# Performance work log

Hardware: AMD Instinct MI355X
Metric: run time of the kernel (lower is better)

## Reference

```python
import jax, jax.numpy as jnp
import numpy as np

N = 50000      # neurons
R = 4          # receptors per neuron
D = 5          # max delay steps
N_IN = 17400   # input (LGN) channels
B = 2
T = 50
E_REC = 2000000
E_IN = 500000
DT = 1.0
SIGMA = 0.5    # gauss_std
DAMP = 0.3     # dampening_factor


@jax.custom_vjp
def spike_gauss(v):
    return (v > 0).astype(v.dtype)

def _sg_fwd(v):
    return (v > 0).astype(v.dtype), v

def _sg_bwd(v, g):
    return (g * jnp.exp(-(v * v) / (SIGMA * SIGMA)) * DAMP,)

spike_gauss.defvjp(_sg_fwd, _sg_bwd)


def _constrained(w):
    # Dale's law: sign buffer is fixed (stop_gradient), values clipped to keep sign
    s = jax.lax.stop_gradient(jnp.sign(w))
    return jnp.where(s >= 0, jax.nn.relu(w), -jax.nn.relu(-w))


def setup_inputs() -> dict:
    ks = jax.random.split(jax.random.key(0), 20)
    x = jax.random.uniform(ks[0], (B, T, N_IN), jnp.float32)
    rest = jax.random.randint(ks[1], (T, B), 0, 11).astype(jnp.int32)  # Binomial(10,0.1) count
    rec_rows = jax.random.randint(ks[2], (E_REC,), 0, R * N).astype(jnp.int32)
    rec_cols = jax.random.randint(ks[3], (E_REC,), 0, D * N).astype(jnp.int32)
    rec_w = jax.random.normal(ks[4], (E_REC,), jnp.float32) * 1e-3
    in_rows = jax.random.randint(ks[5], (E_IN,), 0, R * N).astype(jnp.int32)
    in_cols = jax.random.randint(ks[6], (E_IN,), 0, N_IN).astype(jnp.int32)
    in_w = jax.random.normal(ks[7], (E_IN,), jnp.float32) * 1e-3
    bkg = jax.random.normal(ks[8], (N * R,), jnp.float32) * 0.1
    # per-neuron params, already in normalized voltage units (offset=E_L, scale=V_th-E_L)
    v_th = jnp.ones((N,), jnp.float32)
    e_l = jnp.zeros((N,), jnp.float32)
    v_reset = jax.random.uniform(ks[9], (N,), jnp.float32, -0.2, 0.0)
    g = jax.random.uniform(ks[10], (N,), jnp.float32, 4.0, 6.0)
    c_m = jax.random.uniform(ks[11], (N,), jnp.float32, 100.0, 200.0)
    tau = c_m / g
    decay = jnp.exp(-DT / tau)
    current_factor = (1.0 - decay) * tau / c_m
    t_ref = jnp.full((N,), 2.0, jnp.float32)
    asc_amps = jax.random.normal(ks[12], (N, 2), jnp.float32) * 0.01
    param_k = jax.random.uniform(ks[13], (N, 2), jnp.float32, 0.1, 0.5)
    tau_syn = jax.random.uniform(ks[14], (N, R), jnp.float32, 2.0, 10.0)
    syn_decay = jnp.exp(-DT / tau_syn)
    psc_initial = jnp.asarray(np.e, jnp.float32) / tau_syn
    voltage_scale = jax.random.uniform(ks[15], (N,), jnp.float32, 20.0, 30.0)
    voltage_offset = jnp.full((N,), -70.0, jnp.float32)
    return dict(x=x, rec_w=rec_w, in_w=in_w, bkg=bkg, v_th=v_th, e_l=e_l,
                v_reset=v_reset, g=g, t_ref=t_ref, asc_amps=asc_amps,
                param_k=param_k, decay=decay, current_factor=current_factor,
                syn_decay=syn_decay, psc_initial=psc_initial,
                voltage_scale=voltage_scale, voltage_offset=voltage_offset,
                rec_rows=rec_rows, rec_cols=rec_cols, in_rows=in_rows,
                in_cols=in_cols, rest=rest)


def _forward(x, rec_w, in_w, bkg, v_th, e_l, v_reset, g, t_ref, asc_amps,
             param_k, decay, current_factor, syn_decay, psc_initial,
             voltage_scale, voltage_offset, rec_rows, rec_cols, in_rows,
             in_cols, rest):
    rec_wc = _constrained(rec_w)
    in_wc = _constrained(in_w)
    asc_decay = jnp.exp(-DT * param_k)   # (N,2)
    leak = g * e_l                       # (N,)
    normalizer = v_th - e_l              # (N,)

    z_buf0 = jnp.zeros((B, D, N), jnp.float32)  # delay line, slot 0 = most recent
    v0 = jnp.broadcast_to(v_reset, (B, N))
    zN = jnp.zeros((B, N), jnp.float32)
    zNR = jnp.zeros((B, N, R), jnp.float32)
    carry0 = (z_buf0, v0, zN, zN, zN, zNR, zNR)

    xs = (jnp.transpose(x, (1, 0, 2)), rest)  # (T,B,N_IN), (T,B)

    def step(carry, inp):
        x_t, rest_t = inp
        z_buf, v, r, a1, a2, psc_rise, psc = carry
        # input projection: sparse COO (R*N, N_IN) matvec per batch via gather + scatter-add
        cur = jnp.zeros((B, R * N), jnp.float32).at[:, in_rows].add(x_t[:, in_cols] * in_wc[None, :])
        cur = cur + bkg[None, :] * (rest_t.astype(jnp.float32)[:, None] / 10.0)
        prev_z = z_buf[:, 0]
        zb_flat = z_buf.reshape(B, D * N)
        # recurrent sparse COO (R*N, D*N) matvec over the delay buffer
        i_rec = jnp.zeros((B, R * N), jnp.float32).at[:, rec_rows].add(zb_flat[:, rec_cols] * rec_wc[None, :])
        rec_in = (i_rec + cur).reshape(B, N, R)
        new_psc_rise = syn_decay[None] * psc_rise + rec_in * psc_initial[None]
        new_psc = psc * syn_decay[None] + DT * syn_decay[None] * psc_rise
        new_r = jax.nn.relu(r + prev_z * t_ref[None] - DT)
        new_a1 = asc_decay[:, 0][None] * a1 + prev_z * asc_amps[:, 0][None]
        new_a2 = asc_decay[:, 1][None] * a2 + prev_z * asc_amps[:, 1][None]
        reset_current = prev_z * (v_reset - v_th)[None]
        input_current = psc.sum(-1)  # uses OLD psc, matching the torch code
        new_v = decay[None] * v + current_factor[None] * (input_current + a1 + a2 + leak[None]) + reset_current
        v_sc = (new_v - v_th[None]) / normalizer[None]
        new_z = spike_gauss(v_sc)
        new_z = jnp.where(new_r > 0.0, jnp.zeros_like(new_z), new_z)
        new_z_buf = jnp.concatenate([new_z[:, None, :], z_buf[:, :-1]], axis=1)
        v_out = new_v * voltage_scale[None] + voltage_offset[None]
        new_carry = (new_z_buf, new_v, new_r, new_a1, new_a2, new_psc_rise, new_psc)
        return new_carry, (new_z, v_out)

    _, (zs, vs) = jax.lax.scan(step, carry0, xs)
    return jnp.transpose(zs, (1, 0, 2)), jnp.transpose(vs, (1, 0, 2))  # (B,T,N) each


def reference(x, rec_w, in_w, bkg, v_th, e_l, v_reset, g, t_ref, asc_amps,
              param_k, decay, current_factor, syn_decay, psc_initial,
              voltage_scale, voltage_offset, rec_rows, rec_cols, in_rows,
              in_cols, rest):
    return _forward(x, rec_w, in_w, bkg, v_th, e_l, v_reset, g, t_ref,
                    asc_amps, param_k, decay, current_factor, syn_decay,
                    psc_initial, voltage_scale, voltage_offset, rec_rows,
                    rec_cols, in_rows, in_cols, rest)
```

## Files before the change

kernel.cpp:

```cpp
#include <hip/hip_runtime.h>

#define NN    50000
#define RR    4
#define DDEP  5
#define NIN   17400
#define BB    2
#define TT    50
#define EREC  2000000
#define EIN   500000
#define RNN   (RR*NN)
#define DNN   (DDEP*NN)
#define RING  6
#define TB    (TT*BB)
#define CH    20
#define NCH   (TB/CH)
#define SCAN_TPB 256
#define SCAN_ITEMS 4

struct SP {
  const float* x; const float* bkg;
  const float* v_th; const float* e_l; const float* v_reset; const float* g;
  const float* t_ref; const float* asc_amps; const float* param_k;
  const float* decay; const float* cf; const float* syn_decay; const float* psc_init;
  const float* vscale; const float* voff;
  const int* rest;
  float* out_z; float* out_v;
  float* cur_ring;
  int*   flags;
  int*   bar;
  const int* row_ptr;
  const int2* cw_in;
  const int* col_ptr;
  const int2* cw_rec;
  const float* in_cur;
};

__global__ void hist2_k(const int* __restrict__ in_rows, const int* __restrict__ rec_cols,
                        int* __restrict__ cnt_in, int* __restrict__ cnt_rec) {
  int i = blockIdx.x * blockDim.x + threadIdx.x;
  int nth = gridDim.x * blockDim.x;
  for (int e = i; e < EIN + EREC; e += nth) {
    if (e < EIN) atomicAdd(&cnt_in[in_rows[e]], 1);
    else         atomicAdd(&cnt_rec[rec_cols[e - EIN]], 1);
  }
}

__global__ __launch_bounds__(SCAN_TPB) void blocksum_k(const int* __restrict__ cnt, int n,
                                                       int* __restrict__ partial) {
  __shared__ int sm[SCAN_TPB];
  int base = (blockIdx.x * SCAN_TPB + threadIdx.x) * SCAN_ITEMS;
  int s = 0;
  #pragma unroll
  for (int j = 0; j < SCAN_ITEMS; ++j) { int idx = base + j; if (idx < n) s += cnt[idx]; }
  sm[threadIdx.x] = s; __syncthreads();
  for (int off = SCAN_TPB / 2; off > 0; off >>= 1) {
    if (threadIdx.x < off) sm[threadIdx.x] += sm[threadIdx.x + off];
    __syncthreads();
  }
  if (threadIdx.x == 0) partial[blockIdx.x] = sm[0];
}

__global__ __launch_bounds__(SCAN_TPB) void scanpart_k(int* __restrict__ partial, int nb) {
  __shared__ int sm[SCAN_TPB];
  int i = threadIdx.x;
  int v = (i < nb) ? partial[i] : 0;
  sm[i] = v; __syncthreads();
  for (int off = 1; off < SCAN_TPB; off <<= 1) {
    int a = (i >= off) ? sm[i - off] : 0;
    __syncthreads();
    sm[i] += a;
    __syncthreads();
  }
  if (i < nb) partial[i] = sm[i] - v;
}

__global__ __launch_bounds__(SCAN_TPB) void finalize_k(const int* __restrict__ cnt, int n,
                                                       const int* __restrict__ partial,
                                                       int* __restrict__ ptr,
                                                       int* __restrict__ cursor, int nE) {
  __shared__ int sm[SCAN_TPB];
  int tidl = threadIdx.x;
  int base = (blockIdx.x * SCAN_TPB + tidl) * SCAN_ITEMS;
  int local[SCAN_ITEMS];
  int s = 0;
  #pragma unroll
  for (int j = 0; j < SCAN_ITEMS; ++j) {
    int idx = base + j;
    int c = (idx < n) ? cnt[idx] : 0;
    local[j] = c; s += c;
  }
  sm[tidl] = s; __syncthreads();
  for (int off = 1; off < SCAN_TPB; off <<= 1) {
    int a = (tidl >= off) ? sm[tidl - off] : 0;
    __syncthreads();
    sm[tidl] += a;
    __syncthreads();
  }
  int run = partial[blockIdx.x] + sm[tidl] - s;
  #pragma unroll
  for (int j = 0; j < SCAN_ITEMS; ++j) {
    int idx = base + j;
    if (idx < n) { ptr[idx] = run; cursor[idx] = run; run += local[j]; }
  }
  if (blockIdx.x == 0 && tidl == 0) ptr[n] = nE;
}

__global__ void scatter2_k(const int* __restrict__ in_rows, const int* __restrict__ in_cols,
                           const float* __restrict__ in_w,
                           const int* __restrict__ rec_cols, const int* __restrict__ rec_rows,
                           const float* __restrict__ rec_w,
                           int* __restrict__ cur_in, int* __restrict__ cur_rec,
                           int2* __restrict__ cw_in, int2* __restrict__ cw_rec) {
  int i = blockIdx.x * blockDim.x + threadIdx.x;
  int nth = gridDim.x * blockDim.x;
  for (int e = i; e < EIN + EREC; e += nth) {
    if (e < EIN) {
      int pos = atomicAdd(&cur_in[in_rows[e]], 1);
      cw_in[pos] = make_int2(in_cols[e], __float_as_int(in_w[e]));
    } else {
      int ee = e - EIN;
      int pos = atomicAdd(&cur_rec[rec_cols[ee]], 1);
      cw_rec[pos] = make_int2(rec_rows[ee], __float_as_int(rec_w[ee]));
    }
  }
}

__global__ __launch_bounds__(256) void xpose_k(const float* __restrict__ x,
                                               float* __restrict__ xT) {
  __shared__ float tile[64][TB + 1];
  int c0 = blockIdx.x * 64;
  int cl = threadIdx.x & 63;
  for (int tb = threadIdx.x >> 6; tb < TB; tb += 4) {
    int t = tb >> 1, b = tb & 1;
    int c = c0 + cl;
    tile[cl][tb] = (c < NIN) ? x[((size_t)b * TT + t) * NIN + c] : 0.f;
  }
  __syncthreads();
  int cc = threadIdx.x >> 2;
  int seg = (threadIdx.x & 3) * (TB / 4);
  int c = c0 + cc;
  if (c < NIN) {
    for (int j = seg; j < seg + TB / 4; ++j)
      xT[(size_t)c * TB + j] = tile[cc][j];
  }
}

__global__ __launch_bounds__(256) void precomp2_k(const float* __restrict__ xT,
                                                  const int* __restrict__ rest,
                                                  const float* __restrict__ bkg,
                                                  const int* __restrict__ row_ptr,
                                                  const int2* __restrict__ cw,
                                                  float* __restrict__ ic) {
  const int nbn = (NN + 255) >> 8;
  int chunk = blockIdx.x / nbn;
  int n = (blockIdx.x % nbn) * 256 + threadIdx.x;
  if (n >= NN) return;
  const int tb0 = chunk * CH;

  float restf[CH];
  #pragma unroll
  for (int j = 0; j < CH; ++j) restf[j] = (float)rest[tb0 + j] * 0.1f;

  int rp[RR + 1];
  #pragma unroll
  for (int r = 0; r <= RR; ++r) rp[r] = row_ptr[n * RR + r];

  float acc[RR][CH];
  #pragma unroll
  for (int r = 0; r < RR; ++r) {
    float bk = bkg[n * RR + r];
    #pragma unroll
    for (int j = 0; j < CH; ++j) acc[r][j] = bk * restf[j];
    for (int e = rp[r]; e < rp[r + 1]; ++e) {
      int2 c = cw[e];
      float w = __int_as_float(c.y);
      const float* xr = xT + (size_t)c.x * TB + tb0;
      #pragma unroll
      for (int j = 0; j < CH; ++j) acc[r][j] += w * xr[j];
    }
  }
  #pragma unroll
  for (int j = 0; j < CH; ++j) {
    *(float4*)(ic + (size_t)(tb0 + j) * RNN + (size_t)n * RR) =
        make_float4(acc[0][j], acc[1][j], acc[2][j], acc[3][j]);
  }
}

__device__ __forceinline__ void gridbar(int* bar, int nb, int target) {
  __syncthreads();
  if (threadIdx.x == 0) {
    int* cnt = bar;
    int* gen = bar + 32;
    int old = __hip_atomic_fetch_add(cnt, 1, __ATOMIC_ACQ_REL, __HIP_MEMORY_SCOPE_AGENT);
    if (old == nb - 1) {
      __hip_atomic_store(cnt, 0, __ATOMIC_RELAXED, __HIP_MEMORY_SCOPE_AGENT);
      __hip_atomic_store(gen, target, __ATOMIC_RELEASE, __HIP_MEMORY_SCOPE_AGENT);
    } else {
      while (__hip_atomic_load(gen, __ATOMIC_RELAXED, __HIP_MEMORY_SCOPE_AGENT) < target)
        __builtin_amdgcn_s_sleep(1);
      (void)__hip_atomic_load(gen, __ATOMIC_ACQUIRE, __HIP_MEMORY_SCOPE_AGENT);
    }
  }
  __syncthreads();
}

__global__ __launch_bounds__(1024, 1) void snn_all(SP p) {
  const int tid = blockIdx.x * blockDim.x + threadIdx.x;
  const int nb = gridDim.x;

  const bool owner = tid < BB * NN;
  int b = 0, n = 0;
  float sd[RR], pi[RR], bkgv[RR], psc_rise[RR], psc[RR];
  int rbeg[RR], rend[RR];
  float v = 0.f, refr = 0.f, a1 = 0.f, a2 = 0.f, my_z = 0.f;
  float dcy = 0.f, cfac = 0.f, trf = 0.f, amp1 = 0.f, amp2 = 0.f;
  float ad1 = 0.f, ad2 = 0.f, vth = 0.f, invn = 0.f, leak = 0.f;
  float vrst = 0.f, vsc = 0.f, vof = 0.f;
  #pragma unroll
  for (int r = 0; r < RR; ++r) {
    sd[r]=0.f; pi[r]=0.f; bkgv[r]=0.f; psc_rise[r]=0.f; psc[r]=0.f;
    rbeg[r]=0; rend[r]=0;
  }

  if (owner) {
    b = (tid >= NN) ? 1 : 0;
    n = tid - b * NN;
    #pragma unroll
    for (int r = 0; r < RR; ++r) {
      sd[r] = p.syn_decay[n*RR + r];
      pi[r] = p.psc_init[n*RR + r];
    }
    if (!p.in_cur) {
      #pragma unroll
      for (int r = 0; r < RR; ++r) {
        bkgv[r] = p.bkg[n*RR + r];
        rbeg[r] = p.row_ptr[n*RR + r];
        rend[r] = p.row_ptr[n*RR + r + 1];
      }
    }
    vth  = p.v_th[n];
    float el = p.e_l[n];
    invn = 1.0f / (vth - el);
    leak = p.g[n] * el;
    vrst = p.v_reset[n];
    v    = vrst;
    dcy  = p.decay[n];
    cfac = p.cf[n];
    trf  = p.t_ref[n];
    amp1 = p.asc_amps[2*n+0];
    amp2 = p.asc_amps[2*n+1];
    ad1  = expf(-p.param_k[2*n+0]);
    ad2  = expf(-p.param_k[2*n+1]);
    vsc  = p.vscale[n];
    vof  = p.voff[n];
  }
  const float* xb = p.x + (size_t)b * TT * NIN;
  float* ringB = p.cur_ring + (size_t)b * RING * RNN;

  float4 iv = make_float4(0.f, 0.f, 0.f, 0.f);
  if (owner && p.in_cur)
    iv = *(const float4*)(p.in_cur + (size_t)b * RNN + (size_t)n * RR);

  for (int t = 0; t < TT; ++t) {
    if (t) gridbar(p.bar, nb, t);

    if (owner) {
      int slot = t % RING;
      float4* slotR = (float4*)(ringB + (size_t)slot * RNN);
      float4 rv = slotR[n];
      int flag = p.flags[b*RING + slot];

      float rin[RR];
      if (p.in_cur) {
        rin[0] = iv.x; rin[1] = iv.y; rin[2] = iv.z; rin[3] = iv.w;
        if (t + 1 < TT)
          iv = *(const float4*)(p.in_cur + (size_t)((t+1)*BB + b) * RNN + (size_t)n * RR);
      } else {
        float restf = (float)p.rest[t*BB + b] * 0.1f;
        const float* xt = xb + (size_t)t * NIN;
        #pragma unroll
        for (int r = 0; r < RR; ++r) {
          float acc = bkgv[r] * restf;
          for (int e = rbeg[r]; e < rend[r]; ++e) {
            int2 cw = p.cw_in[e];
            acc += xt[cw.x] * __int_as_float(cw.y);
          }
          rin[r] = acc;
        }
      }

      if (flag == t)
        slotR[n] = make_float4(0.f, 0.f, 0.f, 0.f);
      rin[0] += rv.x; rin[1] += rv.y; rin[2] += rv.z; rin[3] += rv.w;

      float prev_z = my_z;
      float input_current = psc[0] + psc[1] + psc[2] + psc[3];
      float new_v = dcy * v + cfac * (input_current + a1 + a2 + leak)
                    + prev_z * (vrst - vth);
      #pragma unroll
      for (int r = 0; r < RR; ++r) {
        float npsc = psc[r] * sd[r] + sd[r] * psc_rise[r];
        psc_rise[r] = sd[r] * psc_rise[r] + rin[r] * pi[r];
        psc[r] = npsc;
      }
      refr = fmaxf(refr + prev_z * trf - 1.0f, 0.f);
      a1 = ad1 * a1 + prev_z * amp1;
      a2 = ad2 * a2 + prev_z * amp2;
      v = new_v;
      float v_scaled = (new_v - vth) * invn;
      float z = (v_scaled > 0.f) ? 1.f : 0.f;
      if (refr > 0.f) z = 0.f;
      my_z = z;
      size_t oidx = (size_t)b * (TT*NN) + (size_t)t * NN + n;
      p.out_z[oidx] = z;
      p.out_v[oidx] = new_v * vsc + vof;

      if (z != 0.f) {
        #pragma unroll
        for (int d = 0; d < DDEP; ++d) {
          int tt = t + 1 + d;
          if (tt >= TT) break;
          int col = d * NN + n;
          int be = p.col_ptr[col], en = p.col_ptr[col + 1];
          if (be != en) {
            int ws_ = tt % RING;
            p.flags[b*RING + ws_] = tt;
            float* ringW = ringB + (size_t)ws_ * RNN;
            for (int e = be; e < en; ++e) {
              int2 cw = p.cw_rec[e];
              atomicAdd(&ringW[cw.x], __int_as_float(cw.y));
            }
          }
        }
      }
    }
  }
}

extern "C" void kernel_launch(void* const* d_in, const int* in_sizes, int n_in,
                              void* d_out, int out_size, void* d_ws, size_t ws_size,
                              hipStream_t stream) {
  SP p;
  p.x        = (const float*)d_in[0];
  const float* rec_w = (const float*)d_in[1];
  const float* in_w  = (const float*)d_in[2];
  p.bkg      = (const float*)d_in[3];
  p.v_th     = (const float*)d_in[4];
  p.e_l      = (const float*)d_in[5];
  p.v_reset  = (const float*)d_in[6];
  p.g        = (const float*)d_in[7];
  p.t_ref    = (const float*)d_in[8];
  p.asc_amps = (const float*)d_in[9];
  p.param_k  = (const float*)d_in[10];
  p.decay    = (const float*)d_in[11];
  p.cf       = (const float*)d_in[12];
  p.syn_decay= (const float*)d_in[13];
  p.psc_init = (const float*)d_in[14];
  p.vscale   = (const float*)d_in[15];
  p.voff     = (const float*)d_in[16];
  const int* rec_rows = (const int*)d_in[17];
  const int* rec_cols = (const int*)d_in[18];
  const int* in_rows  = (const int*)d_in[19];
  const int* in_cols  = (const int*)d_in[20];
  p.rest     = (const int*)d_in[21];
  p.out_z = (float*)d_out;
  p.out_v = (float*)d_out + (size_t)BB * TT * NN;

  char* ws = (char*)d_ws;
  size_t off = 0;
  auto alloc = [&](size_t bytes) { void* q = ws + off; off += (bytes + 255) & ~(size_t)255; return q; };
  float* cur_ring = (float*)alloc(sizeof(float) * (size_t)BB * RING * RNN);
  int*   flags    = (int*)  alloc(sizeof(int) * BB * RING);
  int*   bar      = (int*)  alloc(sizeof(int) * 64);
  int*   row_ptr  = (int*)  alloc(sizeof(int) * ((size_t)RNN + 1));
  int*   col_ptr  = (int*)  alloc(sizeof(int) * ((size_t)DNN + 1));
  int*   cnt_in   = (int*)  alloc(sizeof(int) * (size_t)RNN);
  int*   cnt_rec  = (int*)  alloc(sizeof(int) * (size_t)DNN);
  int*   cur_in   = (int*)  alloc(sizeof(int) * (size_t)RNN);
  int*   cur_rec  = (int*)  alloc(sizeof(int) * (size_t)DNN);
  int*   part_in  = (int*)  alloc(sizeof(int) * SCAN_TPB);
  int*   part_rec = (int*)  alloc(sizeof(int) * SCAN_TPB);
  int2*  cw_in    = (int2*) alloc(sizeof(int2) * (size_t)EIN);
  int2*  cw_rec   = (int2*) alloc(sizeof(int2) * (size_t)EREC);
  float* xT       = (float*)alloc(sizeof(float) * (size_t)NIN * TB);
  float* in_cur   = (float*)alloc(sizeof(float) * (size_t)TB * RNN);
  const bool use_pre = (off <= ws_size);

  p.cur_ring = cur_ring; p.flags = flags; p.bar = bar;
  p.row_ptr = row_ptr; p.cw_in = cw_in;
  p.col_ptr = col_ptr; p.cw_rec = cw_rec;
  p.in_cur = use_pre ? in_cur : nullptr;

  hipMemsetAsync(cur_ring, 0, sizeof(float) * (size_t)BB * RING * RNN, stream);
  hipMemsetAsync(flags, 0xFF, sizeof(int) * BB * RING, stream);
  hipMemsetAsync(bar, 0, sizeof(int) * 64, stream);
  hipMemsetAsync(cnt_in, 0, sizeof(int) * (size_t)RNN, stream);
  hipMemsetAsync(cnt_rec, 0, sizeof(int) * (size_t)DNN, stream);

  hipLaunchKernelGGL(hist2_k, dim3(1024), dim3(256), 0, stream,
                     in_rows, rec_cols, cnt_in, cnt_rec);

  const int NB_IN  = (RNN + SCAN_TPB * SCAN_ITEMS - 1) / (SCAN_TPB * SCAN_ITEMS);
  const int NB_REC = (DNN + SCAN_TPB * SCAN_ITEMS - 1) / (SCAN_TPB * SCAN_ITEMS);
  hipLaunchKernelGGL(blocksum_k, dim3(NB_IN),  dim3(SCAN_TPB), 0, stream, cnt_in,  RNN, part_in);
  hipLaunchKernelGGL(blocksum_k, dim3(NB_REC), dim3(SCAN_TPB), 0, stream, cnt_rec, DNN, part_rec);
  hipLaunchKernelGGL(scanpart_k, dim3(1), dim3(SCAN_TPB), 0, stream, part_in,  NB_IN);
  hipLaunchKernelGGL(scanpart_k, dim3(1), dim3(SCAN_TPB), 0, stream, part_rec, NB_REC);
  hipLaunchKernelGGL(finalize_k, dim3(NB_IN),  dim3(SCAN_TPB), 0, stream, cnt_in,  RNN, part_in,  row_ptr, cur_in,  EIN);
  hipLaunchKernelGGL(finalize_k, dim3(NB_REC), dim3(SCAN_TPB), 0, stream, cnt_rec, DNN, part_rec, col_ptr, cur_rec, EREC);

  hipLaunchKernelGGL(scatter2_k, dim3(1024), dim3(256), 0, stream,
                     in_rows, in_cols, in_w, rec_cols, rec_rows, rec_w,
                     cur_in, cur_rec, cw_in, cw_rec);

  if (use_pre) {
    hipLaunchKernelGGL(xpose_k, dim3((NIN + 63) / 64), dim3(256), 0, stream, p.x, xT);
    const int nbn = (NN + 255) / 256;
    hipLaunchKernelGGL(precomp2_k, dim3(nbn * NCH), dim3(256), 0, stream,
                       xT, p.rest, p.bkg, row_ptr, cw_in, in_cur);
  }

  void* args[] = { (void*)&p };
  hipLaunchCooperativeKernel(reinterpret_cast<const void*>(&snn_all),
                             dim3(104), dim3(1024), args, 0u, stream);
}
```

Baseline: 841.4 us.

## Use hierarchical tree grid barrier and merge scan/memset launches

Replaces the flat single-counter grid barrier with a two-level tree: eight leaf counters each gather 13 blocks, then leaf leaders meet at a root counter and release their group through per-group generation flags. This is meant to cut atomic contention on one cache line at each of the 49 timestep barriers. It also fuses the paired scan kernels into one launch each using a 2D grid, and merges several memsets into one contiguous memset. The tree adds an extra round-trip of latency per barrier in exchange for less contention.

```diff
diff --git a/kernel.cpp b/kernel.cpp
--- a/kernel.cpp
+++ b/kernel.cpp
@@ -14,6 +14,9 @@
 #define TB    (TT*BB)
 #define CH    20
 #define NCH   (TB/CH)
+#define NBLK  104
+#define NXG   8
+#define GSZ   (NBLK/NXG)
 #define SCAN_TPB 256
 #define SCAN_ITEMS 4
 
@@ -45,8 +48,15 @@
   }
 }
 
-__global__ __launch_bounds__(SCAN_TPB) void blocksum_k(const int* __restrict__ cnt, int n,
-                                                       int* __restrict__ partial) {
+__global__ __launch_bounds__(SCAN_TPB) void blocksum2_k(const int* __restrict__ cnt_in,
+                                                        const int* __restrict__ cnt_rec,
+                                                        int* __restrict__ part_in,
+                                                        int* __restrict__ part_rec) {
+  const int n = blockIdx.y ? DNN : RNN;
+  const int* cnt = blockIdx.y ? cnt_rec : cnt_in;
+  int* partial = blockIdx.y ? part_rec : part_in;
+  const int nb = (n + SCAN_TPB * SCAN_ITEMS - 1) / (SCAN_TPB * SCAN_ITEMS);
+  if ((int)blockIdx.x >= nb) return;
   __shared__ int sm[SCAN_TPB];
   int base = (blockIdx.x * SCAN_TPB + threadIdx.x) * SCAN_ITEMS;
   int s = 0;
@@ -60,7 +70,11 @@
   if (threadIdx.x == 0) partial[blockIdx.x] = sm[0];
 }
 
-__global__ __launch_bounds__(SCAN_TPB) void scanpart_k(int* __restrict__ partial, int nb) {
+__global__ __launch_bounds__(SCAN_TPB) void scanpart2_k(int* __restrict__ part_in,
+                                                        int* __restrict__ part_rec) {
+  const int n = blockIdx.x ? DNN : RNN;
+  int* partial = blockIdx.x ? part_rec : part_in;
+  const int nb = (n + SCAN_TPB * SCAN_ITEMS - 1) / (SCAN_TPB * SCAN_ITEMS);
   __shared__ int sm[SCAN_TPB];
   int i = threadIdx.x;
   int v = (i < nb) ? partial[i] : 0;
@@ -74,10 +88,22 @@
   if (i < nb) partial[i] = sm[i] - v;
 }
 
-__global__ __launch_bounds__(SCAN_TPB) void finalize_k(const int* __restrict__ cnt, int n,
-                                                       const int* __restrict__ partial,
-                                                       int* __restrict__ ptr,
-                                                       int* __restrict__ cursor, int nE) {
+__global__ __launch_bounds__(SCAN_TPB) void finalize2_k(const int* __restrict__ cnt_in,
+                                                        const int* __restrict__ cnt_rec,
+                                                        const int* __restrict__ part_in,
+                                                        const int* __restrict__ part_rec,
+                                                        int* __restrict__ ptr_in,
+                                                        int* __restrict__ ptr_rec,
+                                                        int* __restrict__ cur_in,
+                                                        int* __restrict__ cur_rec) {
+  const int n = blockIdx.y ? DNN : RNN;
+  const int nE = blockIdx.y ? EREC : EIN;
+  const int* cnt = blockIdx.y ? cnt_rec : cnt_in;
+  const int* partial = blockIdx.y ? part_rec : part_in;
+  int* ptr = blockIdx.y ? ptr_rec : ptr_in;
+  int* cursor = blockIdx.y ? cur_rec : cur_in;
+  const int nb = (n + SCAN_TPB * SCAN_ITEMS - 1) / (SCAN_TPB * SCAN_ITEMS);
+  if ((int)blockIdx.x >= nb) return;
   __shared__ int sm[SCAN_TPB];
   int tidl = threadIdx.x;
   int base = (blockIdx.x * SCAN_TPB + tidl) * SCAN_ITEMS;
@@ -186,19 +212,31 @@
   }
 }
 
-__device__ __forceinline__ void gridbar(int* bar, int nb, int target) {
+__device__ __forceinline__ void gridbar(int* bar, int target) {
   __syncthreads();
   if (threadIdx.x == 0) {
-    int* cnt = bar;
-    int* gen = bar + 32;
-    int old = __hip_atomic_fetch_add(cnt, 1, __ATOMIC_ACQ_REL, __HIP_MEMORY_SCOPE_AGENT);
-    if (old == nb - 1) {
-      __hip_atomic_store(cnt, 0, __ATOMIC_RELAXED, __HIP_MEMORY_SCOPE_AGENT);
-      __hip_atomic_store(gen, target, __ATOMIC_RELEASE, __HIP_MEMORY_SCOPE_AGENT);
+    const int g = blockIdx.x & (NXG - 1);
+    int* leafCnt = bar + g * 32;
+    int* rootCnt = bar + NXG * 32;
+    int* rootGen = bar + (NXG + 1) * 32;
+    int* leafGen = bar + (NXG + 2 + g) * 32;
+    int lo = __hip_atomic_fetch_add(leafCnt, 1, __ATOMIC_ACQ_REL, __HIP_MEMORY_SCOPE_AGENT);
+    if (lo == GSZ - 1) {
+      __hip_atomic_store(leafCnt, 0, __ATOMIC_RELAXED, __HIP_MEMORY_SCOPE_AGENT);
+      int ro = __hip_atomic_fetch_add(rootCnt, 1, __ATOMIC_ACQ_REL, __HIP_MEMORY_SCOPE_AGENT);
+      if (ro == NXG - 1) {
+        __hip_atomic_store(rootCnt, 0, __ATOMIC_RELAXED, __HIP_MEMORY_SCOPE_AGENT);
+        __hip_atomic_store(rootGen, target, __ATOMIC_RELEASE, __HIP_MEMORY_SCOPE_AGENT);
+      } else {
+        while (__hip_atomic_load(rootGen, __ATOMIC_RELAXED, __HIP_MEMORY_SCOPE_AGENT) < target)
+          __builtin_amdgcn_s_sleep(1);
+        (void)__hip_atomic_load(rootGen, __ATOMIC_ACQUIRE, __HIP_MEMORY_SCOPE_AGENT);
+      }
+      __hip_atomic_store(leafGen, target, __ATOMIC_RELEASE, __HIP_MEMORY_SCOPE_AGENT);
     } else {
-      while (__hip_atomic_load(gen, __ATOMIC_RELAXED, __HIP_MEMORY_SCOPE_AGENT) < target)
+      while (__hip_atomic_load(leafGen, __ATOMIC_RELAXED, __HIP_MEMORY_SCOPE_AGENT) < target)
         __builtin_amdgcn_s_sleep(1);
-      (void)__hip_atomic_load(gen, __ATOMIC_ACQUIRE, __HIP_MEMORY_SCOPE_AGENT);
+      (void)__hip_atomic_load(leafGen, __ATOMIC_ACQUIRE, __HIP_MEMORY_SCOPE_AGENT);
     }
   }
   __syncthreads();
@@ -206,7 +244,6 @@
 
 __global__ __launch_bounds__(1024, 1) void snn_all(SP p) {
   const int tid = blockIdx.x * blockDim.x + threadIdx.x;
-  const int nb = gridDim.x;
 
   const bool owner = tid < BB * NN;
   int b = 0, n = 0;
@@ -262,7 +299,7 @@
     iv = *(const float4*)(p.in_cur + (size_t)b * RNN + (size_t)n * RR);
 
   for (int t = 0; t < TT; ++t) {
-    if (t) gridbar(p.bar, nb, t);
+    if (t) gridbar(p.bar, t);
 
     if (owner) {
       int slot = t % RING;
@@ -370,12 +407,13 @@
   size_t off = 0;
   auto alloc = [&](size_t bytes) { void* q = ws + off; off += (bytes + 255) & ~(size_t)255; return q; };
   float* cur_ring = (float*)alloc(sizeof(float) * (size_t)BB * RING * RNN);
+  int*   bar      = (int*)  alloc(4096);
+  int*   cnt_in   = (int*)  alloc(sizeof(int) * (size_t)RNN);
+  int*   cnt_rec  = (int*)  alloc(sizeof(int) * (size_t)DNN);
+  size_t zero_end = off;
   int*   flags    = (int*)  alloc(sizeof(int) * BB * RING);
-  int*   bar      = (int*)  alloc(sizeof(int) * 64);
   int*   row_ptr  = (int*)  alloc(sizeof(int) * ((size_t)RNN + 1));
   int*   col_ptr  = (int*)  alloc(sizeof(int) * ((size_t)DNN + 1));
-  int*   cnt_in   = (int*)  alloc(sizeof(int) * (size_t)RNN);
-  int*   cnt_rec  = (int*)  alloc(sizeof(int) * (size_t)DNN);
   int*   cur_in   = (int*)  alloc(sizeof(int) * (size_t)RNN);
   int*   cur_rec  = (int*)  alloc(sizeof(int) * (size_t)DNN);
   int*   part_in  = (int*)  alloc(sizeof(int) * SCAN_TPB);
@@ -391,23 +429,18 @@
   p.col_ptr = col_ptr; p.cw_rec = cw_rec;
   p.in_cur = use_pre ? in_cur : nullptr;
 
-  hipMemsetAsync(cur_ring, 0, sizeof(float) * (size_t)BB * RING * RNN, stream);
+  hipMemsetAsync(ws, 0, zero_end, stream);
   hipMemsetAsync(flags, 0xFF, sizeof(int) * BB * RING, stream);
-  hipMemsetAsync(bar, 0, sizeof(int) * 64, stream);
-  hipMemsetAsync(cnt_in, 0, sizeof(int) * (size_t)RNN, stream);
-  hipMemsetAsync(cnt_rec, 0, sizeof(int) * (size_t)DNN, stream);
 
   hipLaunchKernelGGL(hist2_k, dim3(1024), dim3(256), 0, stream,
                      in_rows, rec_cols, cnt_in, cnt_rec);
 
-  const int NB_IN  = (RNN + SCAN_TPB * SCAN_ITEMS - 1) / (SCAN_TPB * SCAN_ITEMS);
   const int NB_REC = (DNN + SCAN_TPB * SCAN_ITEMS - 1) / (SCAN_TPB * SCAN_ITEMS);
-  hipLaunchKernelGGL(blocksum_k, dim3(NB_IN),  dim3(SCAN_TPB), 0, stream, cnt_in,  RNN, part_in);
-  hipLaunchKernelGGL(blocksum_k, dim3(NB_REC), dim3(SCAN_TPB), 0, stream, cnt_rec, DNN, part_rec);
-  hipLaunchKernelGGL(scanpart_k, dim3(1), dim3(SCAN_TPB), 0, stream, part_in,  NB_IN);
-  hipLaunchKernelGGL(scanpart_k, dim3(1), dim3(SCAN_TPB), 0, stream, part_rec, NB_REC);
-  hipLaunchKernelGGL(finalize_k, dim3(NB_IN),  dim3(SCAN_TPB), 0, stream, cnt_in,  RNN, part_in,  row_ptr, cur_in,  EIN);
-  hipLaunchKernelGGL(finalize_k, dim3(NB_REC), dim3(SCAN_TPB), 0, stream, cnt_rec, DNN, part_rec, col_ptr, cur_rec, EREC);
+  hipLaunchKernelGGL(blocksum2_k, dim3(NB_REC, 2), dim3(SCAN_TPB), 0, stream,
+                     cnt_in, cnt_rec, part_in, part_rec);
+  hipLaunchKernelGGL(scanpart2_k, dim3(2), dim3(SCAN_TPB), 0, stream, part_in, part_rec);
+  hipLaunchKernelGGL(finalize2_k, dim3(NB_REC, 2), dim3(SCAN_TPB), 0, stream,
+                     cnt_in, cnt_rec, part_in, part_rec, row_ptr, col_ptr, cur_in, cur_rec);
 
   hipLaunchKernelGGL(scatter2_k, dim3(1024), dim3(256), 0, stream,
                      in_rows, in_cols, in_w, rec_cols, rec_rows, rec_w,
@@ -422,5 +455,5 @@
 
   void* args[] = { (void*)&p };
   hipLaunchCooperativeKernel(reinterpret_cast<const void*>(&snn_all),
-                             dim3(104), dim3(1024), args, 0u, stream);
-}
+                             dim3(NBLK), dim3(1024), args, 0u, stream);
+}
```

New measurement: 874.4 us. 1.04x slower.
